# Kernel optimization log

Measured on AMD Instinct MI355X. Metric: run time of the kernel, lower is better.

Reference implementation:

```python
import jax, jax.numpy as jnp
import numpy as np

D = 2048
N = 16384
E = 8
THRESHOLD = 0.5


def setup_inputs() -> dict:
    key = jax.random.key(0)
    ks = jax.random.split(key, 6)
    x = jax.random.normal(ks[0], (N, D), dtype=jnp.float32)
    # pretrained weight + truncated SVD basis (frozen in original module)
    W_np = np.asarray(jax.random.normal(ks[1], (D, D), dtype=jnp.float32))
    U, S, Vt = np.linalg.svd(W_np, full_matrices=False)
    k = int((np.cumsum(S) < THRESHOLD * S.sum()).sum())  # energy-threshold rank
    U_k = jnp.asarray(U[:, :k])
    V_k = jnp.asarray(Vt.T[:, :k])  # torch.svd returns V, not V^T
    W = jnp.asarray(W_np)
    lambda_k = jax.random.normal(ks[2], (E, k), dtype=jnp.float32)
    v = jnp.zeros((D,), dtype=jnp.float32)
    W_g1 = jax.random.normal(ks[3], (k, 1), dtype=jnp.float32)
    W_g2 = jax.random.normal(ks[4], (1, E), dtype=jnp.float32)
    return {"x": x, "W": W, "U_k": U_k, "V_k": V_k, "lambda_k": lambda_k,
            "v": v, "W_g1": W_g1, "W_g2": W_g2}


def reference(x, W, U_k, V_k, lambda_k, v, W_g1, W_g2):
    # Routing: g = softmax((x @ U_k) @ W_g1 @ W_g2)  -> [N, E]
    xu = x @ U_k                                   # [N, k] (shared with delta path)
    g = jax.nn.softmax((xu @ W_g1) @ W_g2, axis=-1)
    # sum_i g_i * (x @ (W + U diag(lam_i) V^T))
    #   = (x@W) * sum_i g_i  +  ((x@U) * (g @ lam)) @ V^T   (low-rank factored)
    base = x @ W                                   # [N, D], computed once
    coef = g @ lambda_k                            # [N, k]
    out = base * jnp.sum(g, axis=-1, keepdims=True) + (xu * coef) @ V_k.T
    return out * (1.0 + v)
```

## Files before the change

### kernel.cpp

```cpp
#include <hip/hip_runtime.h>
#include <hip/hip_bf16.h>

#define D_DIM 2048
#define E_DIM 8

typedef __attribute__((ext_vector_type(8))) short short8;
typedef __attribute__((ext_vector_type(4))) float f32x4;

__device__ __forceinline__ unsigned short f2bf(float f) {
  union { float f; unsigned int u; } v; v.f = f;
  unsigned int u = v.u;
  u += 0x7FFFu + ((u >> 16) & 1u);
  return (unsigned short)(u >> 16);
}

__device__ __forceinline__ void async_copy16(const void* g, void* l) {
  __builtin_amdgcn_global_load_lds((const __attribute__((address_space(1))) void*)g,
                                   (__attribute__((address_space(3))) void*)l,
                                   16, 0, 0);
}

__global__ void k_cvt_bf16(const float* __restrict__ in,
                           unsigned short* __restrict__ out, long long n) {
  long long i = ((long long)blockIdx.x * blockDim.x + threadIdx.x) * 8;
  const long long stride = (long long)gridDim.x * blockDim.x * 8;
  for (; i < n; i += stride) {
    float4 a = *(const float4*)(in + i);
    float4 b = *(const float4*)(in + i + 4);
    short8 r;
    r[0] = (short)f2bf(a.x); r[1] = (short)f2bf(a.y);
    r[2] = (short)f2bf(a.z); r[3] = (short)f2bf(a.w);
    r[4] = (short)f2bf(b.x); r[5] = (short)f2bf(b.y);
    r[6] = (short)f2bf(b.z); r[7] = (short)f2bf(b.w);
    *(short8*)(out + i) = r;
  }
}

__global__ void k_transpose_bf16(const float* __restrict__ in, int in_rows, int in_cols,
                                 int in_ld, unsigned short* __restrict__ out, int out_rows) {
  __shared__ float tile[32][33];
  const int tx = threadIdx.x;
  const int ty = threadIdx.y;
  const int c = blockIdx.x * 32 + tx;
  #pragma unroll
  for (int i = 0; i < 4; ++i) {
    const int r = blockIdx.y * 32 + ty + i * 8;
    float vv = 0.0f;
    if (r < in_rows && c < in_cols) vv = in[(size_t)r * in_ld + c];
    tile[ty + i * 8][tx] = vv;
  }
  __syncthreads();
  const int oc = blockIdx.y * 32 + tx;
  #pragma unroll
  for (int i = 0; i < 4; ++i) {
    const int orow = blockIdx.x * 32 + ty + i * 8;
    if (orow < out_rows && oc < in_rows)
      out[(size_t)orow * in_rows + oc] = f2bf(tile[tx][ty + i * 8]);
  }
}

__global__ void k_pad_bf16(const float* __restrict__ in, unsigned short* __restrict__ out,
                           int rows, int cols, int cols_pad) {
  long long idx = (long long)blockIdx.x * blockDim.x + threadIdx.x;
  const long long total = (long long)rows * cols_pad;
  const long long stride = (long long)gridDim.x * blockDim.x;
  for (; idx < total; idx += stride) {
    const int r = (int)(idx / cols_pad);
    const int c = (int)(idx % cols_pad);
    out[idx] = (c < cols) ? f2bf(in[(size_t)r * cols + c]) : (unsigned short)0;
  }
}

__global__ void k_route(const float* __restrict__ xu, int k, int k_pad,
                        const float* __restrict__ Wg1, const float* __restrict__ Wg2,
                        const float* __restrict__ lam,
                        unsigned short* __restrict__ A2, float* __restrict__ rowscale,
                        int Nrows) {
  const int w = threadIdx.x >> 6;
  const int lane = threadIdx.x & 63;
  const int row = blockIdx.x * 4 + w;
  if (row >= Nrows) return;
  const float* xr = xu + (size_t)row * k_pad;
  float s = 0.0f;
  for (int kk = lane; kk < k; kk += 64) s += xr[kk] * Wg1[kk];
  #pragma unroll
  for (int off = 32; off; off >>= 1) s += __shfl_xor(s, off);
  float lg[E_DIM];
  float mx = -INFINITY;
  #pragma unroll
  for (int e = 0; e < E_DIM; ++e) { lg[e] = s * Wg2[e]; mx = fmaxf(mx, lg[e]); }
  float Z = 0.0f;
  #pragma unroll
  for (int e = 0; e < E_DIM; ++e) { lg[e] = expf(lg[e] - mx); Z += lg[e]; }
  float g[E_DIM]; float gsum = 0.0f;
  #pragma unroll
  for (int e = 0; e < E_DIM; ++e) { g[e] = lg[e] / Z; gsum += g[e]; }
  const float inv = 1.0f / gsum;
  if (lane == 0) rowscale[row] = gsum;
  unsigned short* arow = A2 + (size_t)row * k_pad;
  for (int kk = lane; kk < k_pad; kk += 64) {
    if (kk < k) {
      float c = 0.0f;
      #pragma unroll
      for (int e = 0; e < E_DIM; ++e) c += g[e] * lam[(size_t)e * k + kk];
      arow[kk] = f2bf(xr[kk] * (c * inv));
    } else {
      arow[kk] = 0;
    }
  }
}

__global__ __launch_bounds__(256, 2) void k_gemm128(
    const unsigned short* __restrict__ A, long long lda,
    const unsigned short* __restrict__ B, long long ldb,
    int Ktot, float* __restrict__ Cout, int ldc) {
  __shared__ unsigned short lds[4 * 8192];
  const int tid = threadIdx.x;
  const int lane = tid & 63;
  const int w = tid >> 6;
  const long long brow = (long long)blockIdx.x * 128;
  const long long bcol = (long long)blockIdx.y * 128;
  const int c0 = w * 2;
  const int sr0 = lane >> 2;
  const int sj  = lane & 3;
  const int l15 = lane & 15;
  const int jhi = lane >> 4;
  const int wr = (w >> 1) * 64;
  const int wc = (w & 1) * 64;

  auto stage = [&](int tt) {
    unsigned short* dstA = lds + (tt & 3) * 8192;
    #pragma unroll
    for (int c = 0; c < 2; ++c) {
      const int chunk = c0 + c;
      const int lrow = chunk * 16 + sr0;
      const int jj = sj ^ ((lrow >> 1) & 3);
      async_copy16(A + (brow + lrow) * lda + (long long)tt * 32 + jj * 8,
                   (void*)(dstA + chunk * 512));
      async_copy16(B + (bcol + lrow) * ldb + (long long)tt * 32 + jj * 8,
                   (void*)(dstA + 4096 + chunk * 512));
    }
  };

  auto load_frags = [&](int tt, short8* av, short8* bv) {
    const unsigned short* Areg = lds + (tt & 3) * 8192;
    const unsigned short* Breg = Areg + 4096;
    #pragma unroll
    for (int m = 0; m < 4; ++m) {
      const int row = wr + m * 16 + l15;
      const int jj = jhi ^ ((row >> 1) & 3);
      av[m] = *(const short8*)(Areg + row * 32 + jj * 8);
    }
    #pragma unroll
    for (int n = 0; n < 4; ++n) {
      const int row = wc + n * 16 + l15;
      const int jj = jhi ^ ((row >> 1) & 3);
      bv[n] = *(const short8*)(Breg + row * 32 + jj * 8);
    }
  };

  f32x4 acc[4][4];
  #pragma unroll
  for (int m = 0; m < 4; ++m)
    #pragma unroll
    for (int n = 0; n < 4; ++n)
      #pragma unroll
      for (int j = 0; j < 4; ++j) acc[m][n][j] = 0.0f;

  auto do_mfma = [&](short8* av, short8* bv) {
    __builtin_amdgcn_s_setprio(1);
    #pragma unroll
    for (int m = 0; m < 4; ++m)
      #pragma unroll
      for (int n = 0; n < 4; ++n)
        acc[m][n] = __builtin_amdgcn_mfma_f32_16x16x32_bf16(av[m], bv[n], acc[m][n], 0, 0, 0);
    __builtin_amdgcn_s_setprio(0);
  };

  const int NT = Ktot >> 5;
  stage(0); stage(1); stage(2);
  asm volatile("s_waitcnt vmcnt(4)" ::: "memory");
  __builtin_amdgcn_s_barrier();

  short8 avA[4], bvA[4], avB[4], bvB[4];
  load_frags(0, avA, bvA);

  for (int t = 0; t < NT; t += 2) {
    if (t + 3 < NT) stage(t + 3);
    load_frags(t + 1, avB, bvB);
    do_mfma(avA, bvA);
    asm volatile("s_waitcnt vmcnt(4)" ::: "memory");
    __builtin_amdgcn_s_barrier();
    if (t + 4 < NT) stage(t + 4);
    if (t + 2 < NT) load_frags(t + 2, avA, bvA);
    do_mfma(avB, bvB);
    asm volatile("s_waitcnt vmcnt(4)" ::: "memory");
    __builtin_amdgcn_s_barrier();
  }

  #pragma unroll
  for (int m = 0; m < 4; ++m) {
    #pragma unroll
    for (int n = 0; n < 4; ++n) {
      const long long col = bcol + wc + n * 16 + l15;
      #pragma unroll
      for (int j = 0; j < 4; ++j) {
        const long long row = brow + wr + m * 16 + jhi * 4 + j;
        Cout[row * ldc + col] = acc[m][n][j];
      }
    }
  }
}

template<int EPI>
__global__ __launch_bounds__(512, 2) void k_gemm256(
    const unsigned short* __restrict__ A0, int lda0,
    const unsigned short* __restrict__ A1, int lda1,
    const unsigned short* __restrict__ B0, int ldb0,
    const unsigned short* __restrict__ B1, int ldb1,
    int ka0, int Ktot, int gridM,
    float* __restrict__ Cout, int ldc,
    const float* __restrict__ rowscale, const float* __restrict__ vcol) {
  __shared__ unsigned short lds[4 * 16384];
  const int tid = threadIdx.x;
  const int lane = tid & 63;
  const int w = tid >> 6;
  const int wm = w >> 2;
  const int wn = w & 3;

  int bid = blockIdx.x;
  const int cpx = gridDim.x >> 3;
  bid = (bid & 7) * cpx + (bid >> 3);
  const int bx = bid % gridM;
  const int by = bid / gridM;
  const long long brow = (long long)bx * 256;
  const long long bcol = (long long)by * 256;

  const int c0 = w * 2;
  const int sr0 = lane >> 2;
  const int sj  = lane & 3;
  const int l15 = lane & 15;
  const int jhi = lane >> 4;

  auto stage = [&](int tt) {
    const int k0 = tt * 32;
    const unsigned short* PA; long long ldA; long long kA;
    const unsigned short* PB; long long ldB; long long kB;
    if (k0 < ka0) { PA = A0; ldA = lda0; kA = k0;       PB = B0; ldB = ldb0; kB = k0; }
    else          { PA = A1; ldA = lda1; kA = k0 - ka0; PB = B1; ldB = ldb1; kB = k0 - ka0; }
    unsigned short* dst = lds + (tt & 3) * 16384;
    #pragma unroll
    for (int c = 0; c < 2; ++c) {
      const int chunk = c0 + c;
      const int lrow = chunk * 16 + sr0;
      const int jj = sj ^ ((lrow >> 1) & 3);
      async_copy16(PA + (brow + lrow) * ldA + kA + jj * 8, (void*)(dst + chunk * 512));
      async_copy16(PB + (bcol + lrow) * ldB + kB + jj * 8, (void*)(dst + 8192 + chunk * 512));
    }
  };

  auto load_frags = [&](int tt, short8* av, short8* bv) {
    const unsigned short* Areg = lds + (tt & 3) * 16384;
    const unsigned short* Breg = Areg + 8192;
    #pragma unroll
    for (int m = 0; m < 8; ++m) {
      const int row = wm * 128 + m * 16 + l15;
      const int jj = jhi ^ ((row >> 1) & 3);
      av[m] = *(const short8*)(Areg + row * 32 + jj * 8);
    }
    #pragma unroll
    for (int n = 0; n < 4; ++n) {
      const int row = wn * 64 + n * 16 + l15;
      const int jj = jhi ^ ((row >> 1) & 3);
      bv[n] = *(const short8*)(Breg + row * 32 + jj * 8);
    }
  };

  f32x4 acc[8][4];
  #pragma unroll
  for (int m = 0; m < 8; ++m)
    #pragma unroll
    for (int n = 0; n < 4; ++n)
      #pragma unroll
      for (int j = 0; j < 4; ++j) acc[m][n][j] = 0.0f;

  auto do_mfma = [&](short8* av, short8* bv) {
    __builtin_amdgcn_s_setprio(1);
    #pragma unroll
    for (int m = 0; m < 8; ++m)
      #pragma unroll
      for (int n = 0; n < 4; ++n)
        acc[m][n] = __builtin_amdgcn_mfma_f32_16x16x32_bf16(av[m], bv[n], acc[m][n], 0, 0, 0);
    __builtin_amdgcn_s_setprio(0);
  };

  const int NT = Ktot >> 5;
  stage(0); stage(1); stage(2);
  asm volatile("s_waitcnt vmcnt(4)" ::: "memory");
  __builtin_amdgcn_s_barrier();

  short8 avA[8], bvA[4], avB[8], bvB[4];
  load_frags(0, avA, bvA);

  for (int t = 0; t < NT; t += 2) {
    if (t + 3 < NT) stage(t + 3);
    load_frags(t + 1, avB, bvB);
    do_mfma(avA, bvA);
    asm volatile("s_waitcnt vmcnt(4)" ::: "memory");
    __builtin_amdgcn_s_barrier();
    if (t + 4 < NT) stage(t + 4);
    if (t + 2 < NT) load_frags(t + 2, avA, bvA);
    do_mfma(avB, bvB);
    asm volatile("s_waitcnt vmcnt(4)" ::: "memory");
    __builtin_amdgcn_s_barrier();
  }

  #pragma unroll
  for (int m = 0; m < 8; ++m) {
    #pragma unroll
    for (int n = 0; n < 4; ++n) {
      const long long col = bcol + wn * 64 + n * 16 + l15;
      float cs = 1.0f;
      if (EPI == 1) cs = 1.0f + vcol[col];
      #pragma unroll
      for (int j = 0; j < 4; ++j) {
        const long long row = brow + wm * 128 + m * 16 + jhi * 4 + j;
        float val = acc[m][n][j];
        if (EPI == 1) val *= rowscale[row] * cs;
        Cout[row * ldc + col] = val;
      }
    }
  }
}

extern "C" void kernel_launch(void* const* d_in, const int* in_sizes, int n_in,
                              void* d_out, int out_size, void* d_ws, size_t ws_size,
                              hipStream_t stream) {
  const float* x   = (const float*)d_in[0];
  const float* W   = (const float*)d_in[1];
  const float* U   = (const float*)d_in[2];
  const float* V   = (const float*)d_in[3];
  const float* lam = (const float*)d_in[4];
  const float* v   = (const float*)d_in[5];
  const float* Wg1 = (const float*)d_in[6];
  const float* Wg2 = (const float*)d_in[7];
  float* out = (float*)d_out;

  const int N = in_sizes[0] / D_DIM;
  const int k = in_sizes[2] / D_DIM;
  const int k_pad = (k + 127) & ~127;

  char* ws = (char*)d_ws;
  size_t off = 0;
  auto alloc = [&](size_t bytes) -> void* {
    void* p = ws + off;
    off += (bytes + 255) & ~(size_t)255;
    return p;
  };
  unsigned short* xb  = (unsigned short*)alloc((size_t)N * D_DIM * 2);
  unsigned short* Wt  = (unsigned short*)alloc((size_t)D_DIM * D_DIM * 2);
  unsigned short* Ukt = (unsigned short*)alloc((size_t)k_pad * D_DIM * 2);
  unsigned short* Vb  = (unsigned short*)alloc((size_t)D_DIM * k_pad * 2);
  float*          xu  = (float*)alloc((size_t)N * k_pad * 4);
  unsigned short* A2  = (unsigned short*)alloc((size_t)N * k_pad * 2);
  float*          rs  = (float*)alloc((size_t)N * 4);
  if (off > ws_size) return;

  k_cvt_bf16<<<2048, 256, 0, stream>>>(x, xb, (long long)N * D_DIM);
  k_transpose_bf16<<<dim3(D_DIM / 32, D_DIM / 32), dim3(32, 8), 0, stream>>>(
      W, D_DIM, D_DIM, D_DIM, Wt, D_DIM);
  k_transpose_bf16<<<dim3(k_pad / 32, D_DIM / 32), dim3(32, 8), 0, stream>>>(
      U, D_DIM, k, k, Ukt, k_pad);
  k_pad_bf16<<<512, 256, 0, stream>>>(V, Vb, D_DIM, k, k_pad);

  k_gemm128<<<dim3(N / 128, k_pad / 128), 256, 0, stream>>>(
      xb, D_DIM, Ukt, D_DIM, D_DIM, xu, k_pad);

  k_route<<<N / 4, 256, 0, stream>>>(xu, k, k_pad, Wg1, Wg2, lam, A2, rs, N);

  const int gridM = N / 256;
  const int gridN = D_DIM / 256;
  k_gemm256<1><<<gridM * gridN, 512, 0, stream>>>(
      xb, D_DIM, A2, k_pad,
      Wt, D_DIM, Vb, k_pad,
      D_DIM, D_DIM + k_pad, gridM,
      out, D_DIM, rs, v);
}
```

Baseline: 344.4 us.

## Fuse routing coefficients into low-rank GEMM epilogue and gate from x directly

Precomputes u1 = U_k @ W_g1 so a new gate kernel can compute the softmax gates straight from bf16 x. The fp32 xu intermediate and the separate route kernel go away: the x@U_k GEMM now applies g@lambda in its epilogue and writes the bf16 A2 operand directly. The rowscale multiply is dropped because the softmax gates always sum to one. In exchange, the gate kernel re-reads all of x, and the small GEMM moves to a 2-stage LDS pipeline that waits on vmcnt(0) every step, traded for higher occupancy.

Result: faster. 327.8 us (-4.8%).

```diff
diff --git a/kernel.cpp b/kernel.cpp
--- a/kernel.cpp
+++ b/kernel.cpp
@@ -12,6 +12,11 @@
   unsigned int u = v.u;
   u += 0x7FFFu + ((u >> 16) & 1u);
   return (unsigned short)(u >> 16);
+}
+
+__device__ __forceinline__ float bf2f(unsigned short h) {
+  union { unsigned int u; float f; } v; v.u = ((unsigned int)h) << 16;
+  return v.f;
 }
 
 __device__ __forceinline__ void async_copy16(const void* g, void* l) {
@@ -71,50 +76,62 @@
   }
 }
 
-__global__ void k_route(const float* __restrict__ xu, int k, int k_pad,
-                        const float* __restrict__ Wg1, const float* __restrict__ Wg2,
-                        const float* __restrict__ lam,
-                        unsigned short* __restrict__ A2, float* __restrict__ rowscale,
-                        int Nrows) {
+__global__ void k_u1(const float* __restrict__ U, const float* __restrict__ Wg1,
+                     float* __restrict__ u1, int D, int k) {
+  const int w = threadIdx.x >> 6;
+  const int lane = threadIdx.x & 63;
+  const int d = blockIdx.x * 4 + w;
+  if (d >= D) return;
+  const float* row = U + (size_t)d * k;
+  float s = 0.0f;
+  for (int j = lane; j < k; j += 64) s += row[j] * Wg1[j];
+  #pragma unroll
+  for (int off = 32; off; off >>= 1) s += __shfl_xor(s, off);
+  if (lane == 0) u1[d] = s;
+}
+
+__global__ void k_gate(const unsigned short* __restrict__ xb,
+                       const float* __restrict__ u1, const float* __restrict__ Wg2,
+                       float* __restrict__ g8, int Nrows) {
   const int w = threadIdx.x >> 6;
   const int lane = threadIdx.x & 63;
   const int row = blockIdx.x * 4 + w;
   if (row >= Nrows) return;
-  const float* xr = xu + (size_t)row * k_pad;
+  const unsigned short* xr = xb + (size_t)row * D_DIM;
   float s = 0.0f;
-  for (int kk = lane; kk < k; kk += 64) s += xr[kk] * Wg1[kk];
+  #pragma unroll
+  for (int t = 0; t < D_DIM / 512; ++t) {
+    const int base = (t * 64 + lane) * 8;
+    short8 v = *(const short8*)(xr + base);
+    float4 ua = *(const float4*)(u1 + base);
+    float4 ub = *(const float4*)(u1 + base + 4);
+    s += bf2f((unsigned short)v[0]) * ua.x + bf2f((unsigned short)v[1]) * ua.y +
+         bf2f((unsigned short)v[2]) * ua.z + bf2f((unsigned short)v[3]) * ua.w +
+         bf2f((unsigned short)v[4]) * ub.x + bf2f((unsigned short)v[5]) * ub.y +
+         bf2f((unsigned short)v[6]) * ub.z + bf2f((unsigned short)v[7]) * ub.w;
+  }
   #pragma unroll
   for (int off = 32; off; off >>= 1) s += __shfl_xor(s, off);
-  float lg[E_DIM];
-  float mx = -INFINITY;
-  #pragma unroll
-  for (int e = 0; e < E_DIM; ++e) { lg[e] = s * Wg2[e]; mx = fmaxf(mx, lg[e]); }
-  float Z = 0.0f;
-  #pragma unroll
-  for (int e = 0; e < E_DIM; ++e) { lg[e] = expf(lg[e] - mx); Z += lg[e]; }
-  float g[E_DIM]; float gsum = 0.0f;
-  #pragma unroll
-  for (int e = 0; e < E_DIM; ++e) { g[e] = lg[e] / Z; gsum += g[e]; }
-  const float inv = 1.0f / gsum;
-  if (lane == 0) rowscale[row] = gsum;
-  unsigned short* arow = A2 + (size_t)row * k_pad;
-  for (int kk = lane; kk < k_pad; kk += 64) {
-    if (kk < k) {
-      float c = 0.0f;
-      #pragma unroll
-      for (int e = 0; e < E_DIM; ++e) c += g[e] * lam[(size_t)e * k + kk];
-      arow[kk] = f2bf(xr[kk] * (c * inv));
-    } else {
-      arow[kk] = 0;
-    }
-  }
-}
-
-__global__ __launch_bounds__(256, 2) void k_gemm128(
+  if (lane == 0) {
+    float lg[E_DIM], mx = -INFINITY;
+    #pragma unroll
+    for (int e = 0; e < E_DIM; ++e) { lg[e] = s * Wg2[e]; mx = fmaxf(mx, lg[e]); }
+    float Z = 0.0f;
+    #pragma unroll
+    for (int e = 0; e < E_DIM; ++e) { lg[e] = expf(lg[e] - mx); Z += lg[e]; }
+    const float inv = 1.0f / Z;
+    #pragma unroll
+    for (int e = 0; e < E_DIM; ++e) g8[(size_t)row * E_DIM + e] = lg[e] * inv;
+  }
+}
+
+__global__ __launch_bounds__(256, 3) void k_gemm128(
     const unsigned short* __restrict__ A, long long lda,
     const unsigned short* __restrict__ B, long long ldb,
-    int Ktot, float* __restrict__ Cout, int ldc) {
-  __shared__ unsigned short lds[4 * 8192];
+    int Ktot,
+    const float* __restrict__ g8, const float* __restrict__ lam, int k_real,
+    unsigned short* __restrict__ A2, int lda2) {
+  __shared__ unsigned short lds[2 * 8192];
   const int tid = threadIdx.x;
   const int lane = tid & 63;
   const int w = tid >> 6;
@@ -129,7 +146,7 @@
   const int wc = (w & 1) * 64;
 
   auto stage = [&](int tt) {
-    unsigned short* dstA = lds + (tt & 3) * 8192;
+    unsigned short* dstA = lds + (tt & 1) * 8192;
     #pragma unroll
     for (int c = 0; c < 2; ++c) {
       const int chunk = c0 + c;
@@ -142,9 +159,24 @@
     }
   };
 
-  auto load_frags = [&](int tt, short8* av, short8* bv) {
-    const unsigned short* Areg = lds + (tt & 3) * 8192;
+  f32x4 acc[4][4];
+  #pragma unroll
+  for (int m = 0; m < 4; ++m)
+    #pragma unroll
+    for (int n = 0; n < 4; ++n)
+      #pragma unroll
+      for (int j = 0; j < 4; ++j) acc[m][n][j] = 0.0f;
+
+  const int NT = Ktot >> 5;
+  stage(0);
+  asm volatile("s_waitcnt vmcnt(0)" ::: "memory");
+  __builtin_amdgcn_s_barrier();
+
+  for (int t = 0; t < NT; ++t) {
+    const unsigned short* Areg = lds + (t & 1) * 8192;
     const unsigned short* Breg = Areg + 4096;
+    if (t + 1 < NT) stage(t + 1);
+    short8 av[4], bv[4];
     #pragma unroll
     for (int m = 0; m < 4; ++m) {
       const int row = wr + m * 16 + l15;
@@ -157,11 +189,122 @@
       const int jj = jhi ^ ((row >> 1) & 3);
       bv[n] = *(const short8*)(Breg + row * 32 + jj * 8);
     }
+    __builtin_amdgcn_s_setprio(1);
+    #pragma unroll
+    for (int m = 0; m < 4; ++m)
+      #pragma unroll
+      for (int n = 0; n < 4; ++n)
+        acc[m][n] = __builtin_amdgcn_mfma_f32_16x16x32_bf16(av[m], bv[n], acc[m][n], 0, 0, 0);
+    __builtin_amdgcn_s_setprio(0);
+    asm volatile("s_waitcnt vmcnt(0)" ::: "memory");
+    __builtin_amdgcn_s_barrier();
+  }
+
+  float lamE[E_DIM][4];
+  #pragma unroll
+  for (int n = 0; n < 4; ++n) {
+    const long long col = bcol + wc + n * 16 + l15;
+    #pragma unroll
+    for (int e = 0; e < E_DIM; ++e)
+      lamE[e][n] = (col < k_real) ? lam[(size_t)e * k_real + col] : 0.0f;
+  }
+  #pragma unroll
+  for (int m = 0; m < 4; ++m) {
+    float coef[4][4];
+    #pragma unroll
+    for (int j = 0; j < 4; ++j)
+      #pragma unroll
+      for (int n = 0; n < 4; ++n) coef[j][n] = 0.0f;
+    #pragma unroll
+    for (int j = 0; j < 4; ++j) {
+      const long long row = brow + wr + m * 16 + jhi * 4 + j;
+      const float* gr = g8 + row * E_DIM;
+      #pragma unroll
+      for (int e = 0; e < E_DIM; ++e) {
+        const float ge = gr[e];
+        #pragma unroll
+        for (int n = 0; n < 4; ++n) coef[j][n] += ge * lamE[e][n];
+      }
+    }
+    #pragma unroll
+    for (int n = 0; n < 4; ++n) {
+      const long long col = bcol + wc + n * 16 + l15;
+      #pragma unroll
+      for (int j = 0; j < 4; ++j) {
+        const long long row = brow + wr + m * 16 + jhi * 4 + j;
+        A2[row * lda2 + col] = f2bf(acc[m][n][j] * coef[j][n]);
+      }
+    }
+  }
+}
+
+template<int EPI>
+__global__ __launch_bounds__(512, 2) void k_gemm256(
+    const unsigned short* __restrict__ A0, int lda0,
+    const unsigned short* __restrict__ A1, int lda1,
+    const unsigned short* __restrict__ B0, int ldb0,
+    const unsigned short* __restrict__ B1, int ldb1,
+    int ka0, int Ktot, int gridM,
+    float* __restrict__ Cout, int ldc,
+    const float* __restrict__ vcol) {
+  __shared__ unsigned short lds[4 * 16384];
+  const int tid = threadIdx.x;
+  const int lane = tid & 63;
+  const int w = tid >> 6;
+  const int wm = w >> 2;
+  const int wn = w & 3;
+
+  int bid = blockIdx.x;
+  const int cpx = gridDim.x >> 3;
+  bid = (bid & 7) * cpx + (bid >> 3);
+  const int bx = bid % gridM;
+  const int by = bid / gridM;
+  const long long brow = (long long)bx * 256;
+  const long long bcol = (long long)by * 256;
+
+  const int c0 = w * 2;
+  const int sr0 = lane >> 2;
+  const int sj  = lane & 3;
+  const int l15 = lane & 15;
+  const int jhi = lane >> 4;
+
+  auto stage = [&](int tt) {
+    const int k0 = tt * 32;
+    const unsigned short* PA; long long ldA; long long kA;
+    const unsigned short* PB; long long ldB; long long kB;
+    if (k0 < ka0) { PA = A0; ldA = lda0; kA = k0;       PB = B0; ldB = ldb0; kB = k0; }
+    else          { PA = A1; ldA = lda1; kA = k0 - ka0; PB = B1; ldB = ldb1; kB = k0 - ka0; }
+    unsigned short* dst = lds + (tt & 3) * 16384;
+    #pragma unroll
+    for (int c = 0; c < 2; ++c) {
+      const int chunk = c0 + c;
+      const int lrow = chunk * 16 + sr0;
+      const int jj = sj ^ ((lrow >> 1) & 3);
+      async_copy16(PA + (brow + lrow) * ldA + kA + jj * 8, (void*)(dst + chunk * 512));
+      async_copy16(PB + (bcol + lrow) * ldB + kB + jj * 8, (void*)(dst + 8192 + chunk * 512));
+    }
   };
 
-  f32x4 acc[4][4];
-  #pragma unroll
-  for (int m = 0; m < 4; ++m)
+  auto load_frags = [&](int tt, short8* av, short8* bv) {
+    const unsigned short* Areg = lds + (tt & 3) * 16384;
+    const unsigned short* Breg = Areg + 8192;
+    #pragma unroll
+    for (int m = 0; m < 8; ++m) {
+      const int row = wm * 128 + m * 16 + l15;
+      const int jj = jhi ^ ((row >> 1) & 3);
+      av[m] = *(const short8*)(Areg + row * 32 + jj * 8);
+    }
+    #pragma unroll
+    for (int n = 0; n < 4; ++n) {
+      const int row = wn * 64 + n * 16 + l15;
+      const int jj = jhi ^ ((row >> 1) & 3);
+      bv[n] = *(const short8*)(Breg + row * 32 + jj * 8);
+    }
+  };
+
+  f32x4 acc[8][4];
+  #pragma unroll
+  for (int m = 0; m < 8; ++m)
     #pragma unroll
     for (int n = 0; n < 4; ++n)
       #pragma unroll
@@ -170,7 +313,7 @@
   auto do_mfma = [&](short8* av, short8* bv) {
     __builtin_amdgcn_s_setprio(1);
     #pragma unroll
-    for (int m = 0; m < 4; ++m)
+    for (int m = 0; m < 8; ++m)
       #pragma unroll
       for (int n = 0; n < 4; ++n)
         acc[m][n] = __builtin_amdgcn_mfma_f32_16x16x32_bf16(av[m], bv[n], acc[m][n], 0, 0, 0);
@@ -182,7 +325,7 @@
   asm volatile("s_waitcnt vmcnt(4)" ::: "memory");
   __builtin_amdgcn_s_barrier();
 
-  short8 avA[4], bvA[4], avB[4], bvB[4];
+  short8 avA[8], bvA[4], avB[8], bvB[4];
   load_frags(0, avA, bvA);
 
   for (int t = 0; t < NT; t += 2) {
@@ -199,123 +342,6 @@
   }
 
   #pragma unroll
-  for (int m = 0; m < 4; ++m) {
-    #pragma unroll
-    for (int n = 0; n < 4; ++n) {
-      const long long col = bcol + wc + n * 16 + l15;
-      #pragma unroll
-      for (int j = 0; j < 4; ++j) {
-        const long long row = brow + wr + m * 16 + jhi * 4 + j;
-        Cout[row * ldc + col] = acc[m][n][j];
-      }
-    }
-  }
-}
-
-template<int EPI>
-__global__ __launch_bounds__(512, 2) void k_gemm256(
-    const unsigned short* __restrict__ A0, int lda0,
-    const unsigned short* __restrict__ A1, int lda1,
-    const unsigned short* __restrict__ B0, int ldb0,
-    const unsigned short* __restrict__ B1, int ldb1,
-    int ka0, int Ktot, int gridM,
-    float* __restrict__ Cout, int ldc,
-    const float* __restrict__ rowscale, const float* __restrict__ vcol) {
-  __shared__ unsigned short lds[4 * 16384];
-  const int tid = threadIdx.x;
-  const int lane = tid & 63;
-  const int w = tid >> 6;
-  const int wm = w >> 2;
-  const int wn = w & 3;
-
-  int bid = blockIdx.x;
-  const int cpx = gridDim.x >> 3;
-  bid = (bid & 7) * cpx + (bid >> 3);
-  const int bx = bid % gridM;
-  const int by = bid / gridM;
-  const long long brow = (long long)bx * 256;
-  const long long bcol = (long long)by * 256;
-
-  const int c0 = w * 2;
-  const int sr0 = lane >> 2;
-  const int sj  = lane & 3;
-  const int l15 = lane & 15;
-  const int jhi = lane >> 4;
-
-  auto stage = [&](int tt) {
-    const int k0 = tt * 32;
-    const unsigned short* PA; long long ldA; long long kA;
-    const unsigned short* PB; long long ldB; long long kB;
-    if (k0 < ka0) { PA = A0; ldA = lda0; kA = k0;       PB = B0; ldB = ldb0; kB = k0; }
-    else          { PA = A1; ldA = lda1; kA = k0 - ka0; PB = B1; ldB = ldb1; kB = k0 - ka0; }
-    unsigned short* dst = lds + (tt & 3) * 16384;
-    #pragma unroll
-    for (int c = 0; c < 2; ++c) {
-      const int chunk = c0 + c;
-      const int lrow = chunk * 16 + sr0;
-      const int jj = sj ^ ((lrow >> 1) & 3);
-      async_copy16(PA + (brow + lrow) * ldA + kA + jj * 8, (void*)(dst + chunk * 512));
-      async_copy16(PB + (bcol + lrow) * ldB + kB + jj * 8, (void*)(dst + 8192 + chunk * 512));
-    }
-  };
-
-  auto load_frags = [&](int tt, short8* av, short8* bv) {
-    const unsigned short* Areg = lds + (tt & 3) * 16384;
-    const unsigned short* Breg = Areg + 8192;
-    #pragma unroll
-    for (int m = 0; m < 8; ++m) {
-      const int row = wm * 128 + m * 16 + l15;
-      const int jj = jhi ^ ((row >> 1) & 3);
-      av[m] = *(const short8*)(Areg + row * 32 + jj * 8);
-    }
-    #pragma unroll
-    for (int n = 0; n < 4; ++n) {
-      const int row = wn * 64 + n * 16 + l15;
-      const int jj = jhi ^ ((row >> 1) & 3);
-      bv[n] = *(const short8*)(Breg + row * 32 + jj * 8);
-    }
-  };
-
-  f32x4 acc[8][4];
-  #pragma unroll
-  for (int m = 0; m < 8; ++m)
-    #pragma unroll
-    for (int n = 0; n < 4; ++n)
-      #pragma unroll
-      for (int j = 0; j < 4; ++j) acc[m][n][j] = 0.0f;
-
-  auto do_mfma = [&](short8* av, short8* bv) {
-    __builtin_amdgcn_s_setprio(1);
-    #pragma unroll
-    for (int m = 0; m < 8; ++m)
-      #pragma unroll
-      for (int n = 0; n < 4; ++n)
-        acc[m][n] = __builtin_amdgcn_mfma_f32_16x16x32_bf16(av[m], bv[n], acc[m][n], 0, 0, 0);
-    __builtin_amdgcn_s_setprio(0);
-  };
-
-  const int NT = Ktot >> 5;
-  stage(0); stage(1); stage(2);
-  asm volatile("s_waitcnt vmcnt(4)" ::: "memory");
-  __builtin_amdgcn_s_barrier();
-
-  short8 avA[8], bvA[4], avB[8], bvB[4];
-  load_frags(0, avA, bvA);
-
-  for (int t = 0; t < NT; t += 2) {
-    if (t + 3 < NT) stage(t + 3);
-    load_frags(t + 1, avB, bvB);
-    do_mfma(avA, bvA);
-    asm volatile("s_waitcnt vmcnt(4)" ::: "memory");
-    __builtin_amdgcn_s_barrier();
-    if (t + 4 < NT) stage(t + 4);
-    if (t + 2 < NT) load_frags(t + 2, avA, bvA);
-    do_mfma(avB, bvB);
-    asm volatile("s_waitcnt vmcnt(4)" ::: "memory");
-    __builtin_amdgcn_s_barrier();
-  }
-
-  #pragma unroll
   for (int m = 0; m < 8; ++m) {
     #pragma unroll
     for (int n = 0; n < 4; ++n) {
@@ -325,9 +351,7 @@
       #pragma unroll
       for (int j = 0; j < 4; ++j) {
         const long long row = brow + wm * 128 + m * 16 + jhi * 4 + j;
-        float val = acc[m][n][j];
-        if (EPI == 1) val *= rowscale[row] * cs;
-        Cout[row * ldc + col] = val;
+        Cout[row * ldc + col] = acc[m][n][j] * cs;
       }
     }
   }
@@ -361,9 +385,9 @@
   unsigned short* Wt  = (unsigned short*)alloc((size_t)D_DIM * D_DIM * 2);
   unsigned short* Ukt = (unsigned short*)alloc((size_t)k_pad * D_DIM * 2);
   unsigned short* Vb  = (unsigned short*)alloc((size_t)D_DIM * k_pad * 2);
-  float*          xu  = (float*)alloc((size_t)N * k_pad * 4);
   unsigned short* A2  = (unsigned short*)alloc((size_t)N * k_pad * 2);
-  float*          rs  = (float*)alloc((size_t)N * 4);
+  float*          u1  = (float*)alloc((size_t)D_DIM * 4);
+  float*          g8  = (float*)alloc((size_t)N * E_DIM * 4);
   if (off > ws_size) return;
 
   k_cvt_bf16<<<2048, 256, 0, stream>>>(x, xb, (long long)N * D_DIM);
@@ -372,11 +396,12 @@
   k_transpose_bf16<<<dim3(k_pad / 32, D_DIM / 32), dim3(32, 8), 0, stream>>>(
       U, D_DIM, k, k, Ukt, k_pad);
   k_pad_bf16<<<512, 256, 0, stream>>>(V, Vb, D_DIM, k, k_pad);
+  k_u1<<<D_DIM / 4, 256, 0, stream>>>(U, Wg1, u1, D_DIM, k);
+
+  k_gate<<<N / 4, 256, 0, stream>>>(xb, u1, Wg2, g8, N);
 
   k_gemm128<<<dim3(N / 128, k_pad / 128), 256, 0, stream>>>(
-      xb, D_DIM, Ukt, D_DIM, D_DIM, xu, k_pad);
-
-  k_route<<<N / 4, 256, 0, stream>>>(xu, k, k_pad, Wg1, Wg2, lam, A2, rs, N);
+      xb, D_DIM, Ukt, D_DIM, D_DIM, g8, lam, k, A2, k_pad);
 
   const int gridM = N / 256;
   const int gridN = D_DIM / 256;
@@ -384,5 +409,5 @@
       xb, D_DIM, A2, k_pad,
       Wt, D_DIM, Vb, k_pad,
       D_DIM, D_DIM + k_pad, gridM,
-      out, D_DIM, rs, v);
-}
+      out, D_DIM, v);
+}
```
